# Kernel tuning notes

Hardware: AMD Instinct MI355X
Metric: run time of the kernel (lower is better)

Reference implementation:

```python
import jax, jax.numpy as jnp
import numpy as np


def setup_inputs() -> dict:
    key = jax.random.key(0)
    ks = jax.random.split(key, 9)
    B, F, D = 512, 32, 64
    units = [128, 128, 128]
    inp = {
        "x": jax.random.normal(ks[0], (B, F, D), dtype=jnp.float32),
        "W0": jax.random.normal(ks[1], (units[0], F * F), dtype=jnp.float32) * 0.02,
        "b0": jax.random.normal(ks[2], (units[0],), dtype=jnp.float32) * 0.02,
        "W1": jax.random.normal(ks[3], (units[1], units[0] * F), dtype=jnp.float32) * 0.02,
        "b1": jax.random.normal(ks[4], (units[1],), dtype=jnp.float32) * 0.02,
        "W2": jax.random.normal(ks[5], (units[2], units[1] * F), dtype=jnp.float32) * 0.02,
        "b2": jax.random.normal(ks[6], (units[2],), dtype=jnp.float32) * 0.02,
        "Wout": jax.random.normal(ks[7], (sum(units), 1), dtype=jnp.float32) * 0.02,
        "bout": jax.random.normal(ks[8], (1,), dtype=jnp.float32) * 0.02,
    }
    return inp


def reference(x, W0, b0, W1, b1, W2, b2, Wout, bout):
    # x: [B, F, D]
    B, F, D = x.shape
    x0 = x[:, :, None, :]  # [B, F, 1, D]
    h = x                   # [B, H, D], H starts at F
    outs = []
    for W, b in ((W0, b0), (W1, b1), (W2, b2)):
        # outer product over field dims: [B, F, H, D]
        z = x0 * h[:, None, :, :]
        Bn, Fd, Hd, Dd = z.shape
        z = z.reshape(Bn, Fd * Hd, Dd)  # channels = f*H + h (torch view order)
        # 1x1 Conv1d == matmul over channels: [B, C_in, D] x [C_out, C_in]
        y = jnp.einsum('bcd,oc->bod', z, W) + b[None, :, None]  # [B, U, D]
        h = y
        outs.append(y.sum(axis=2))  # [B, U]
    out = jnp.concatenate(outs, axis=1)       # [B, sum(units)]
    out = jax.nn.relu(out)
    out = out @ Wout + bout                    # [B, 1]
    return jax.nn.sigmoid(out)
```

## Files before the change

kernel.cpp:

```cpp
#include <hip/hip_runtime.h>
#include <math.h>


typedef __attribute__((ext_vector_type(8))) _Float16 f16x8;
typedef __attribute__((ext_vector_type(4))) _Float16 f16x4;
typedef __attribute__((ext_vector_type(4))) float f32x4;
typedef __attribute__((ext_vector_type(4))) unsigned short u16x4;

__device__ __forceinline__ unsigned short f2h(float f) {
  union { _Float16 h; unsigned short u; } c; c.h = (_Float16)f; return c.u;
}

__device__ __forceinline__ void gll16(const void* g, void* l) {
  __builtin_amdgcn_global_load_lds(
      (const __attribute__((address_space(1))) unsigned int*)g,
      (__attribute__((address_space(3))) unsigned int*)l, 16, 0, 0);
}

__global__ void repack_w_all(const float* __restrict__ W0q, const float* __restrict__ W1q,
                             const float* __restrict__ W2q,
                             unsigned short* __restrict__ D0, unsigned short* __restrict__ D1,
                             unsigned short* __restrict__ D2)
{
  const int blk = blockIdx.x;
  const float* W; unsigned short* dst; int H, t;
  if (blk < 64)       { W = W0q; dst = D0; H = 32;  t = blk * 256 + threadIdx.x; }
  else if (blk < 320) { W = W1q; dst = D1; H = 128; t = (blk - 64) * 256 + threadIdx.x; }
  else                { W = W2q; dst = D2; H = 128; t = (blk - 320) * 256 + threadIdx.x; }
  const int K = 32 * H;
  const int idx = t & 511;
  const int c   = t >> 9;
  const int pass = c >> 5, f = c & 31;
  const int mt = idx >> 6, l = idx & 63;
  const int o = mt * 16 + (l & 15);
  const int kcol = f * H + pass * 32 + ((l >> 4) & 3) * 8;
  const float* s = W + (size_t)o * K + kcol;
  u16x4 a, bq;
#pragma unroll
  for (int j = 0; j < 4; ++j) {
    a[j]  = f2h(s[j]);
    bq[j] = f2h(s[4 + j]);
  }
  *(u16x4*)(dst + (size_t)t * 8)     = a;
  *(u16x4*)(dst + (size_t)t * 8 + 4) = bq;
}

#define BODY(SPOFF, Ac, Ad, Ap)                                                 \
  {                                                                             \
    const f16x4 sv0 = *(const f16x4*)(xp0 + (SPOFF));                           \
    const f16x4 sv1 = *(const f16x4*)(xp1 + (SPOFF));                           \
    const f16x8 z00 = Bh0[0] * sv0[0];                                          \
    const f16x8 z01 = Bh0[1] * sv0[1];                                          \
    const f16x8 z02 = Bh0[2] * sv0[2];                                          \
    const f16x8 z03 = Bh0[3] * sv0[3];                                          \
    const f16x8 z10 = Bh1[0] * sv1[0];                                          \
    const f16x8 z11 = Bh1[1] * sv1[1];                                          \
    const f16x8 z12 = Bh1[2] * sv1[2];                                          \
    const f16x8 z13 = Bh1[3] * sv1[3];                                          \
    Y0[0] = __builtin_amdgcn_mfma_f32_16x16x32_f16(Ac, z00, Y0[0], 0, 0, 0);    \
    Y1[0] = __builtin_amdgcn_mfma_f32_16x16x32_f16(Ac, z10, Y1[0], 0, 0, 0);    \
    Y0[1] = __builtin_amdgcn_mfma_f32_16x16x32_f16(Ac, z01, Y0[1], 0, 0, 0);    \
    Y1[1] = __builtin_amdgcn_mfma_f32_16x16x32_f16(Ac, z11, Y1[1], 0, 0, 0);    \
    Y0[2] = __builtin_amdgcn_mfma_f32_16x16x32_f16(Ac, z02, Y0[2], 0, 0, 0);    \
    Y1[2] = __builtin_amdgcn_mfma_f32_16x16x32_f16(Ac, z12, Y1[2], 0, 0, 0);    \
    Y0[3] = __builtin_amdgcn_mfma_f32_16x16x32_f16(Ac, z03, Y0[3], 0, 0, 0);    \
    Y1[3] = __builtin_amdgcn_mfma_f32_16x16x32_f16(Ac, z13, Y1[3], 0, 0, 0);    \
    Ad = Ap[0];                                                                 \
    Ap += 1024;                                                                 \
  }

template<int H, int NPASS, bool FIRST, bool STORE_H, bool FINAL>
__global__ __launch_bounds__(512, 2) void cin_mfma_layer(
    const unsigned short* __restrict__ Wimg,
    const float* __restrict__ x,
    const unsigned short* __restrict__ hTin,
    const float* __restrict__ bias,
    unsigned short* __restrict__ hTout,
    float* __restrict__ outs, int col_off,
    const float* __restrict__ Wout,
    const float* __restrict__ bout,
    float* __restrict__ out)
{
  __shared__ char lds[24576];
  const int tid = threadIdx.x;
  const int w = tid >> 6, l = tid & 63, g = l >> 4, li = l & 15;
  const int b0 = blockIdx.x * 2;
  const float* lx0 = (const float*)lds;
  const float* lx1 = (const float*)(lds + 8192);
  const _Float16* xt0 = (const _Float16*)(lds + 16384);
  const _Float16* xt1 = (const _Float16*)(lds + 20480);

  gll16(x + (size_t)b0 * 2048 + tid * 4,       lds + w * 1024);
  gll16(x + (size_t)(b0 + 1) * 2048 + tid * 4, lds + 8192 + w * 1024);

  f32x4 Y0[4], Y1[4];
#pragma unroll
  for (int nt = 0; nt < 4; ++nt) {
    Y0[nt] = (f32x4){0.f, 0.f, 0.f, 0.f};
    Y1[nt] = (f32x4){0.f, 0.f, 0.f, 0.f};
  }
  f16x8 Bh0[4], Bh1[4];

  asm volatile("s_waitcnt vmcnt(0)" ::: "memory");
  __builtin_amdgcn_s_barrier();

  {
    const int tf = tid >> 4, tl = tid & 15;
    f16x4 v0, v1;
#pragma unroll
    for (int q = 0; q < 4; ++q) {
      v0[q] = (_Float16)lx0[tf * 64 + q * 16 + tl];
      v1[q] = (_Float16)lx1[tf * 64 + q * 16 + tl];
    }
    *(f16x4*)(lds + 16384 + (tf * 16 + tl) * 8) = v0;
    *(f16x4*)(lds + 20480 + (tf * 16 + tl) * 8) = v1;
  }
  __builtin_amdgcn_s_barrier();

  if constexpr (FIRST) {
#pragma unroll
    for (int nt = 0; nt < 4; ++nt) {
      union { f16x8 v; _Float16 u[8]; } t0, t1;
#pragma unroll
      for (int j = 0; j < 8; ++j) {
        t0.u[j] = (_Float16)lx0[(g * 8 + j) * 64 + nt * 16 + li];
        t1.u[j] = (_Float16)lx1[(g * 8 + j) * 64 + nt * 16 + li];
      }
      Bh0[nt] = t0.v; Bh1[nt] = t1.v;
    }
  }

  const f16x8* Abase = (const f16x8*)Wimg + (w * 64 + l);
  f16x8 Aa = Abase[0];
  f16x8 Ab = Abase[512];
  const f16x8* ApA = Abase + 1024;
  const f16x8* ApB = Abase + 1536;

  for (int pass = 0; pass < NPASS; ++pass) {
    if constexpr (!FIRST) {
#pragma unroll
      for (int nt = 0; nt < 4; ++nt) {
        const size_t co = (size_t)(nt * 16 + li) * 128 + pass * 32 + g * 8;
        Bh0[nt] = *(const f16x8*)(hTin + (size_t)b0 * 8192 + co);
        Bh1[nt] = *(const f16x8*)(hTin + (size_t)(b0 + 1) * 8192 + co);
      }
    }
    const _Float16* xp0 = xt0 + li * 4;
    const _Float16* xp1 = xt1 + li * 4;
#pragma unroll 1
    for (int fo = 0; fo < 32; fo += 2) {
      BODY(0,  Aa, Aa, ApA)
      BODY(64, Ab, Ab, ApB)
      xp0 += 128;
      xp1 += 128;
    }
  }

  const f32x4 bv = *(const f32x4*)(bias + w * 16 + g * 4);
#pragma unroll
  for (int nt = 0; nt < 4; ++nt) { Y0[nt] += bv; Y1[nt] += bv; }

  if constexpr (STORE_H) {
#pragma unroll
    for (int nt = 0; nt < 4; ++nt) {
      const int d = nt * 16 + li;
      u16x4 p0, p1;
#pragma unroll
      for (int j = 0; j < 4; ++j) { p0[j] = f2h(Y0[nt][j]); p1[j] = f2h(Y1[nt][j]); }
      const size_t co = (size_t)d * 128 + w * 16 + g * 4;
      *(u16x4*)(hTout + (size_t)b0 * 8192 + co)       = p0;
      *(u16x4*)(hTout + (size_t)(b0 + 1) * 8192 + co) = p1;
    }
  }

  f32x4 s0 = Y0[0] + Y0[1] + Y0[2] + Y0[3];
  f32x4 s1 = Y1[0] + Y1[1] + Y1[2] + Y1[3];
#pragma unroll
  for (int m = 1; m < 16; m <<= 1) {
    s0.x += __shfl_xor(s0.x, m, 16); s0.y += __shfl_xor(s0.y, m, 16);
    s0.z += __shfl_xor(s0.z, m, 16); s0.w += __shfl_xor(s0.w, m, 16);
    s1.x += __shfl_xor(s1.x, m, 16); s1.y += __shfl_xor(s1.y, m, 16);
    s1.z += __shfl_xor(s1.z, m, 16); s1.w += __shfl_xor(s1.w, m, 16);
  }

  if constexpr (FINAL) {
    __builtin_amdgcn_s_barrier();
    float* shs = (float*)lds;
    if (li == 0) {
      *(f32x4*)(shs + w * 16 + g * 4)       = s0;
      *(f32x4*)(shs + 128 + w * 16 + g * 4) = s1;
    }
    __builtin_amdgcn_s_barrier();
    if (w < 2) {
      const int bb = b0 + w;
      const float* sh = shs + w * 128;
      float acc;
      {
        float v0 = sh[l];      v0 = v0 > 0.f ? v0 : 0.f;
        float v1 = sh[l + 64]; v1 = v1 > 0.f ? v1 : 0.f;
        acc = v0 * Wout[256 + l] + v1 * Wout[320 + l];
      }
#pragma unroll
      for (int q = 0; q < 4; ++q) {
        float v = outs[(size_t)bb * 256 + q * 64 + l];
        v = v > 0.f ? v : 0.f;
        acc = fmaf(v, Wout[q * 64 + l], acc);
      }
#pragma unroll
      for (int m = 32; m; m >>= 1) acc += __shfl_xor(acc, m, 64);
      if (l == 0) {
        const float t = acc + bout[0];
        out[bb] = 1.f / (1.f + expf(-t));
      }
    }
  } else {
    if (li == 0) {
      *(f32x4*)(outs + (size_t)b0 * 256 + col_off + w * 16 + g * 4)       = s0;
      *(f32x4*)(outs + (size_t)(b0 + 1) * 256 + col_off + w * 16 + g * 4) = s1;
    }
  }
}

extern "C" void kernel_launch(void* const* d_in, const int* in_sizes, int n_in,
                              void* d_out, int out_size, void* d_ws, size_t ws_size,
                              hipStream_t stream)
{
  const float* x    = (const float*)d_in[0];
  const float* W0   = (const float*)d_in[1];
  const float* b0   = (const float*)d_in[2];
  const float* W1   = (const float*)d_in[3];
  const float* b1   = (const float*)d_in[4];
  const float* W2   = (const float*)d_in[5];
  const float* b2   = (const float*)d_in[6];
  const float* Wout = (const float*)d_in[7];
  const float* bout = (const float*)d_in[8];
  float* out = (float*)d_out;

  char* ws = (char*)d_ws;
  unsigned short* hT1  = (unsigned short*)ws;
  unsigned short* hT2  = (unsigned short*)(ws + (8 << 20));
  float*          outs = (float*)        (ws + (16 << 20));
  unsigned short* Wi0  = (unsigned short*)(ws + (17 << 20));
  unsigned short* Wi1  = (unsigned short*)(ws + (17 << 20) + (1 << 19));
  unsigned short* Wi2  = (unsigned short*)(ws + (19 << 20));

  repack_w_all<<<576, 256, 0, stream>>>(W0, W1, W2, Wi0, Wi1, Wi2);

  cin_mfma_layer<32,  1, true,  true,  false><<<256, 512, 0, stream>>>(
      Wi0, x, nullptr, b0, hT1, outs, 0, nullptr, nullptr, nullptr);
  cin_mfma_layer<128, 4, false, true,  false><<<256, 512, 0, stream>>>(
      Wi1, x, hT1, b1, hT2, outs, 128, nullptr, nullptr, nullptr);
  cin_mfma_layer<128, 4, false, false, true ><<<256, 512, 0, stream>>>(
      Wi2, x, hT2, b2, nullptr, outs, 0, Wout, bout, out);
}
```

Before: 107.8 us.

## Switch CIN layers to 32x32x16 MFMA tiles with repacked weights

Replaces the 16x16x32 MFMA tiling with 32x32x16 instructions. Each wave now covers 32 output units by 32 embedding columns, and the weight repack layout changes to match the new A-operand fragments. Per MFMA it cuts the x scalar loads and broadcast multiplies and raises arithmetic per operand fetch. The cost is a longer 64-lane shuffle reduction and an extra LDS pass plus two barriers to combine the two d-halves of the row sums.

```diff
diff --git a/kernel.cpp b/kernel.cpp
--- a/kernel.cpp
+++ b/kernel.cpp
@@ -2,10 +2,11 @@
 #include <math.h>
 
 
-typedef __attribute__((ext_vector_type(8))) _Float16 f16x8;
-typedef __attribute__((ext_vector_type(4))) _Float16 f16x4;
-typedef __attribute__((ext_vector_type(4))) float f32x4;
-typedef __attribute__((ext_vector_type(4))) unsigned short u16x4;
+typedef __attribute__((ext_vector_type(8)))  _Float16 f16x8;
+typedef __attribute__((ext_vector_type(4)))  _Float16 f16x4;
+typedef __attribute__((ext_vector_type(4)))  float f32x4;
+typedef __attribute__((ext_vector_type(16))) float f32x16;
+typedef __attribute__((ext_vector_type(4)))  unsigned short u16x4;
 
 __device__ __forceinline__ unsigned short f2h(float f) {
   union { _Float16 h; unsigned short u; } c; c.h = (_Float16)f; return c.u;
@@ -28,12 +29,12 @@
   else if (blk < 320) { W = W1q; dst = D1; H = 128; t = (blk - 64) * 256 + threadIdx.x; }
   else                { W = W2q; dst = D2; H = 128; t = (blk - 320) * 256 + threadIdx.x; }
   const int K = 32 * H;
-  const int idx = t & 511;
-  const int c   = t >> 9;
+  const int c = t >> 9;
+  const int r = t & 511;
+  const int ks = r >> 8, mt = (r >> 6) & 3, l = r & 63;
   const int pass = c >> 5, f = c & 31;
-  const int mt = idx >> 6, l = idx & 63;
-  const int o = mt * 16 + (l & 15);
-  const int kcol = f * H + pass * 32 + ((l >> 4) & 3) * 8;
+  const int o = mt * 32 + (l & 31);
+  const int kcol = f * H + pass * 32 + ks * 16 + (l >> 5) * 8;
   const float* s = W + (size_t)o * K + kcol;
   u16x4 a, bq;
 #pragma unroll
@@ -45,27 +46,21 @@
   *(u16x4*)(dst + (size_t)t * 8 + 4) = bq;
 }
 
-#define BODY(SPOFF, Ac, Ad, Ap)                                                 \
+#define BODY(A0, A1, Ad0, Ad1, Ap)                                              \
   {                                                                             \
-    const f16x4 sv0 = *(const f16x4*)(xp0 + (SPOFF));                           \
-    const f16x4 sv1 = *(const f16x4*)(xp1 + (SPOFF));                           \
-    const f16x8 z00 = Bh0[0] * sv0[0];                                          \
-    const f16x8 z01 = Bh0[1] * sv0[1];                                          \
-    const f16x8 z02 = Bh0[2] * sv0[2];                                          \
-    const f16x8 z03 = Bh0[3] * sv0[3];                                          \
-    const f16x8 z10 = Bh1[0] * sv1[0];                                          \
-    const f16x8 z11 = Bh1[1] * sv1[1];                                          \
-    const f16x8 z12 = Bh1[2] * sv1[2];                                          \
-    const f16x8 z13 = Bh1[3] * sv1[3];                                          \
-    Y0[0] = __builtin_amdgcn_mfma_f32_16x16x32_f16(Ac, z00, Y0[0], 0, 0, 0);    \
-    Y1[0] = __builtin_amdgcn_mfma_f32_16x16x32_f16(Ac, z10, Y1[0], 0, 0, 0);    \
-    Y0[1] = __builtin_amdgcn_mfma_f32_16x16x32_f16(Ac, z01, Y0[1], 0, 0, 0);    \
-    Y1[1] = __builtin_amdgcn_mfma_f32_16x16x32_f16(Ac, z11, Y1[1], 0, 0, 0);    \
-    Y0[2] = __builtin_amdgcn_mfma_f32_16x16x32_f16(Ac, z02, Y0[2], 0, 0, 0);    \
-    Y1[2] = __builtin_amdgcn_mfma_f32_16x16x32_f16(Ac, z12, Y1[2], 0, 0, 0);    \
-    Y0[3] = __builtin_amdgcn_mfma_f32_16x16x32_f16(Ac, z03, Y0[3], 0, 0, 0);    \
-    Y1[3] = __builtin_amdgcn_mfma_f32_16x16x32_f16(Ac, z13, Y1[3], 0, 0, 0);    \
-    Ad = Ap[0];                                                                 \
+    const _Float16 s0 = *xp0;                                                   \
+    const _Float16 s1 = *xp1;                                                   \
+    xp0 += 64; xp1 += 64;                                                       \
+    const f16x8 z00 = Bh0[0] * s0;                                              \
+    const f16x8 z01 = Bh0[1] * s0;                                              \
+    const f16x8 z10 = Bh1[0] * s1;                                              \
+    const f16x8 z11 = Bh1[1] * s1;                                              \
+    Y0 = __builtin_amdgcn_mfma_f32_32x32x16_f16(A0, z00, Y0, 0, 0, 0);          \
+    Y1 = __builtin_amdgcn_mfma_f32_32x32x16_f16(A0, z10, Y1, 0, 0, 0);          \
+    Y0 = __builtin_amdgcn_mfma_f32_32x32x16_f16(A1, z01, Y0, 0, 0, 0);          \
+    Y1 = __builtin_amdgcn_mfma_f32_32x32x16_f16(A1, z11, Y1, 0, 0, 0);          \
+    Ad0 = Ap[0];                                                                \
+    Ad1 = Ap[256];                                                              \
     Ap += 1024;                                                                 \
   }
 
@@ -81,119 +76,129 @@
     const float* __restrict__ bout,
     float* __restrict__ out)
 {
-  __shared__ char lds[24576];
+  __shared__ char lds[25600];
   const int tid = threadIdx.x;
-  const int w = tid >> 6, l = tid & 63, g = l >> 4, li = l & 15;
+  const int w = tid >> 6, l = tid & 63, lo5 = l & 31, hi = l >> 5;
+  const int mt = w & 3, dt = w >> 2;
+  const int dt32 = dt * 32;
   const int b0 = blockIdx.x * 2;
   const float* lx0 = (const float*)lds;
   const float* lx1 = (const float*)(lds + 8192);
-  const _Float16* xt0 = (const _Float16*)(lds + 16384);
-  const _Float16* xt1 = (const _Float16*)(lds + 20480);
+  const _Float16* xs0 = (const _Float16*)(lds + 16384);
+  const _Float16* xs1 = (const _Float16*)(lds + 20480);
 
   gll16(x + (size_t)b0 * 2048 + tid * 4,       lds + w * 1024);
   gll16(x + (size_t)(b0 + 1) * 2048 + tid * 4, lds + 8192 + w * 1024);
 
-  f32x4 Y0[4], Y1[4];
-#pragma unroll
-  for (int nt = 0; nt < 4; ++nt) {
-    Y0[nt] = (f32x4){0.f, 0.f, 0.f, 0.f};
-    Y1[nt] = (f32x4){0.f, 0.f, 0.f, 0.f};
-  }
-  f16x8 Bh0[4], Bh1[4];
+  f32x16 Y0 = {}, Y1 = {};
+  f16x8 Bh0[2], Bh1[2];
 
   asm volatile("s_waitcnt vmcnt(0)" ::: "memory");
   __builtin_amdgcn_s_barrier();
 
   {
-    const int tf = tid >> 4, tl = tid & 15;
-    f16x4 v0, v1;
-#pragma unroll
-    for (int q = 0; q < 4; ++q) {
-      v0[q] = (_Float16)lx0[tf * 64 + q * 16 + tl];
-      v1[q] = (_Float16)lx1[tf * 64 + q * 16 + tl];
-    }
-    *(f16x4*)(lds + 16384 + (tf * 16 + tl) * 8) = v0;
-    *(f16x4*)(lds + 20480 + (tf * 16 + tl) * 8) = v1;
-  }
-  __builtin_amdgcn_s_barrier();
+    const f32x4 v0 = *(const f32x4*)(lx0 + tid * 4);
+    const f32x4 v1 = *(const f32x4*)(lx1 + tid * 4);
+    f16x4 h0, h1;
+#pragma unroll
+    for (int q = 0; q < 4; ++q) { h0[q] = (_Float16)v0[q]; h1[q] = (_Float16)v1[q]; }
+    *(f16x4*)(lds + 16384 + tid * 8) = h0;
+    *(f16x4*)(lds + 20480 + tid * 8) = h1;
+  }
+  __syncthreads();
 
   if constexpr (FIRST) {
 #pragma unroll
-    for (int nt = 0; nt < 4; ++nt) {
+    for (int ks = 0; ks < 2; ++ks) {
       union { f16x8 v; _Float16 u[8]; } t0, t1;
 #pragma unroll
       for (int j = 0; j < 8; ++j) {
-        t0.u[j] = (_Float16)lx0[(g * 8 + j) * 64 + nt * 16 + li];
-        t1.u[j] = (_Float16)lx1[(g * 8 + j) * 64 + nt * 16 + li];
-      }
-      Bh0[nt] = t0.v; Bh1[nt] = t1.v;
-    }
-  }
-
-  const f16x8* Abase = (const f16x8*)Wimg + (w * 64 + l);
-  f16x8 Aa = Abase[0];
-  f16x8 Ab = Abase[512];
+        const int fr = ks * 16 + hi * 8 + j;
+        t0.u[j] = (_Float16)lx0[fr * 64 + dt32 + lo5];
+        t1.u[j] = (_Float16)lx1[fr * 64 + dt32 + lo5];
+      }
+      Bh0[ks] = t0.v; Bh1[ks] = t1.v;
+    }
+  }
+
+  const f16x8* Abase = (const f16x8*)Wimg + (mt * 64 + l);
+  f16x8 Aa0 = Abase[0],   Aa1 = Abase[256];
+  f16x8 Ab0 = Abase[512], Ab1 = Abase[768];
   const f16x8* ApA = Abase + 1024;
   const f16x8* ApB = Abase + 1536;
 
   for (int pass = 0; pass < NPASS; ++pass) {
     if constexpr (!FIRST) {
-#pragma unroll
-      for (int nt = 0; nt < 4; ++nt) {
-        const size_t co = (size_t)(nt * 16 + li) * 128 + pass * 32 + g * 8;
-        Bh0[nt] = *(const f16x8*)(hTin + (size_t)b0 * 8192 + co);
-        Bh1[nt] = *(const f16x8*)(hTin + (size_t)(b0 + 1) * 8192 + co);
-      }
-    }
-    const _Float16* xp0 = xt0 + li * 4;
-    const _Float16* xp1 = xt1 + li * 4;
+      const int d = dt32 + lo5;
+#pragma unroll
+      for (int ks = 0; ks < 2; ++ks) {
+        const size_t co = (size_t)d * 128 + pass * 32 + ks * 16 + hi * 8;
+        Bh0[ks] = *(const f16x8*)(hTin + (size_t)b0 * 8192 + co);
+        Bh1[ks] = *(const f16x8*)(hTin + (size_t)(b0 + 1) * 8192 + co);
+      }
+    }
+    const _Float16* xp0 = xs0 + dt32 + lo5;
+    const _Float16* xp1 = xs1 + dt32 + lo5;
 #pragma unroll 1
-    for (int fo = 0; fo < 32; fo += 2) {
-      BODY(0,  Aa, Aa, ApA)
-      BODY(64, Ab, Ab, ApB)
-      xp0 += 128;
-      xp1 += 128;
-    }
-  }
-
-  const f32x4 bv = *(const f32x4*)(bias + w * 16 + g * 4);
-#pragma unroll
-  for (int nt = 0; nt < 4; ++nt) { Y0[nt] += bv; Y1[nt] += bv; }
+    for (int i = 0; i < 32; i += 2) {
+      BODY(Aa0, Aa1, Aa0, Aa1, ApA)
+      BODY(Ab0, Ab1, Ab0, Ab1, ApB)
+    }
+  }
+
+#pragma unroll
+  for (int q = 0; q < 4; ++q) {
+    const f32x4 bq = *(const f32x4*)(bias + mt * 32 + q * 8 + hi * 4);
+#pragma unroll
+    for (int j = 0; j < 4; ++j) { Y0[q * 4 + j] += bq[j]; Y1[q * 4 + j] += bq[j]; }
+  }
 
   if constexpr (STORE_H) {
-#pragma unroll
-    for (int nt = 0; nt < 4; ++nt) {
-      const int d = nt * 16 + li;
+    const int d = dt32 + lo5;
+#pragma unroll
+    for (int q = 0; q < 4; ++q) {
       u16x4 p0, p1;
 #pragma unroll
-      for (int j = 0; j < 4; ++j) { p0[j] = f2h(Y0[nt][j]); p1[j] = f2h(Y1[nt][j]); }
-      const size_t co = (size_t)d * 128 + w * 16 + g * 4;
+      for (int j = 0; j < 4; ++j) { p0[j] = f2h(Y0[q * 4 + j]); p1[j] = f2h(Y1[q * 4 + j]); }
+      const size_t co = (size_t)d * 128 + mt * 32 + q * 8 + hi * 4;
       *(u16x4*)(hTout + (size_t)b0 * 8192 + co)       = p0;
       *(u16x4*)(hTout + (size_t)(b0 + 1) * 8192 + co) = p1;
     }
   }
 
-  f32x4 s0 = Y0[0] + Y0[1] + Y0[2] + Y0[3];
-  f32x4 s1 = Y1[0] + Y1[1] + Y1[2] + Y1[3];
-#pragma unroll
-  for (int m = 1; m < 16; m <<= 1) {
-    s0.x += __shfl_xor(s0.x, m, 16); s0.y += __shfl_xor(s0.y, m, 16);
-    s0.z += __shfl_xor(s0.z, m, 16); s0.w += __shfl_xor(s0.w, m, 16);
-    s1.x += __shfl_xor(s1.x, m, 16); s1.y += __shfl_xor(s1.y, m, 16);
-    s1.z += __shfl_xor(s1.z, m, 16); s1.w += __shfl_xor(s1.w, m, 16);
-  }
+  f32x16 S0 = Y0, S1 = Y1;
+#pragma unroll
+  for (int m = 1; m < 32; m <<= 1)
+#pragma unroll
+    for (int q = 0; q < 16; ++q) {
+      S0[q] += __shfl_xor(S0[q], m, 64);
+      S1[q] += __shfl_xor(S1[q], m, 64);
+    }
+
+  float* sums = (float*)(lds + 24576);
+  if (dt == 0 && lo5 == 0) {
+#pragma unroll
+    for (int q = 0; q < 16; ++q) {
+      const int o = mt * 32 + (q & 3) + 8 * (q >> 2) + 4 * hi;
+      sums[o]       = S0[q];
+      sums[128 + o] = S1[q];
+    }
+  }
+  __syncthreads();
+  if (dt == 1 && lo5 == 0) {
+#pragma unroll
+    for (int q = 0; q < 16; ++q) {
+      const int o = mt * 32 + (q & 3) + 8 * (q >> 2) + 4 * hi;
+      sums[o]       += S0[q];
+      sums[128 + o] += S1[q];
+    }
+  }
+  __syncthreads();
 
   if constexpr (FINAL) {
-    __builtin_amdgcn_s_barrier();
-    float* shs = (float*)lds;
-    if (li == 0) {
-      *(f32x4*)(shs + w * 16 + g * 4)       = s0;
-      *(f32x4*)(shs + 128 + w * 16 + g * 4) = s1;
-    }
-    __builtin_amdgcn_s_barrier();
     if (w < 2) {
       const int bb = b0 + w;
-      const float* sh = shs + w * 128;
+      const float* sh = sums + w * 128;
       float acc;
       {
         float v0 = sh[l];      v0 = v0 > 0.f ? v0 : 0.f;
@@ -214,9 +219,9 @@
       }
     }
   } else {
-    if (li == 0) {
-      *(f32x4*)(outs + (size_t)b0 * 256 + col_off + w * 16 + g * 4)       = s0;
-      *(f32x4*)(outs + (size_t)(b0 + 1) * 256 + col_off + w * 16 + g * 4) = s1;
+    if (tid < 256) {
+      const int bb = tid >> 7, col = tid & 127;
+      outs[(size_t)(b0 + bb) * 256 + col_off + col] = sums[bb * 128 + col];
     }
   }
 }
```

Result: no change. 108.2 us (+0.4%).
